# Performance work log

Measured on AMD Instinct MI355X. Metric: run time of the kernel, lower is better.

Reference implementation:

```python
import jax, jax.numpy as jnp
import numpy as np

NEG = -1e6  # masked_softmax fill value from the torch source


def setup_inputs() -> dict:
    key = jax.random.key(0)
    ks = jax.random.split(key, 7)
    B, NQ, NK, D, H = 4, 256, 1024, 256, 256
    queries = jax.random.normal(ks[0], (B, NQ, D), dtype=jnp.float32)
    keys_ = jax.random.normal(ks[1], (B, NK, D), dtype=jnp.float32)
    values = jax.random.normal(ks[2], (B, NK, D), dtype=jnp.float32)
    valid_lens = jax.random.randint(ks[3], (B,), 1, NK + 1, dtype=jnp.int32)
    scale = 1.0 / np.sqrt(D)
    Wq = jax.random.normal(ks[4], (D, H), dtype=jnp.float32) * scale
    Wk = jax.random.normal(ks[5], (D, H), dtype=jnp.float32) * scale
    w_v = jax.random.normal(ks[6], (H,), dtype=jnp.float32) * (1.0 / np.sqrt(H))
    return {"queries": queries, "keys": keys_, "values": values,
            "valid_lens": valid_lens, "Wq": Wq, "Wk": Wk, "w_v": w_v}


def reference(queries, keys, values, valid_lens, Wq, Wk, w_v):
    # projections
    q = jnp.einsum('bqd,dh->bqh', queries, Wq)           # [B,NQ,H]
    k = jnp.einsum('bkd,dh->bkh', keys, Wk)              # [B,NK,H]
    # broadcast-add + tanh + dense(->1): scores [B,NQ,NK]
    features = jnp.tanh(q[:, :, None, :] + k[:, None, :, :])  # [B,NQ,NK,H]
    scores = jnp.einsum('bqkh,h->bqk', features, w_v)
    # masked softmax over last axis with per-batch valid lengths
    nk = keys.shape[1]
    mask = jnp.arange(nk)[None, None, :] < valid_lens[:, None, None]  # [B,1,NK]
    scores = jnp.where(mask, scores, NEG)
    attn = jax.nn.softmax(scores, axis=-1)               # [B,NQ,NK]
    # dropout in eval mode -> identity
    return jnp.einsum('bqk,bkd->bqd', attn, values)      # [B,NQ,D]
```

## Files before the change

kernel.cpp:

```cpp
#include <hip/hip_runtime.h>
#include <hip/hip_fp16.h>
#include <math.h>

#define BB 4
#define NQ 256
#define NK 1024
#define DD 256
#define HH 256

typedef __attribute__((ext_vector_type(8))) _Float16 f16x8;
typedef __attribute__((ext_vector_type(4))) _Float16 f16x4;
typedef __attribute__((ext_vector_type(4))) float f32x4;

__global__ __launch_bounds__(256) void proj_mfma_kernel(
    const float* __restrict__ Q, const float* __restrict__ K,
    const float* __restrict__ Wq, const float* __restrict__ Wk,
    const int* __restrict__ vlen,
    __half* __restrict__ Eq, __half* __restrict__ Ek)
{
    int bx = blockIdx.x;
    int mt = bx >> 3, nt = bx & 7;
    const float *A, *W; __half* C; int bm;
    if (mt < 16) { A = Q; W = Wq; C = Eq; bm = mt * 64; }
    else {
        int kt = mt - 16;
        int b = kt >> 4;
        int lr = (kt & 15) * 64;
        if (lr >= vlen[b]) return;
        A = K; W = Wk; C = Ek; bm = kt * 64;
    }
    int bn = nt * 32;

    __shared__ __half Wt[32][260];

    int tid = threadIdx.x;
    {
        int dp = tid >> 3, cg = tid & 7;
#pragma unroll
        for (int pp = 0; pp < 4; ++pp) {
            int d0r = (dp + pp * 32) * 2;
            float4 r0 = *(const float4*)&W[(size_t)d0r * HH + bn + cg * 4];
            float4 r1 = *(const float4*)&W[(size_t)(d0r + 1) * HH + bn + cg * 4];
            int n = cg * 4;
            *(__half2*)&Wt[n + 0][d0r] = __floats2half2_rn(r0.x, r1.x);
            *(__half2*)&Wt[n + 1][d0r] = __floats2half2_rn(r0.y, r1.y);
            *(__half2*)&Wt[n + 2][d0r] = __floats2half2_rn(r0.z, r1.z);
            *(__half2*)&Wt[n + 3][d0r] = __floats2half2_rn(r0.w, r1.w);
        }
    }
    __syncthreads();

    int lane = tid & 63, w = tid >> 6;
    int wm = w & 1, wn = w >> 1;
    int lm = lane & 15, lk = (lane >> 4) * 4;

    const float* arow0 = A + (size_t)(bm + wm * 32 + lm) * DD;
    const float* arow1 = arow0 + (size_t)16 * DD;
    const __half* brow = &Wt[wn * 16 + lm][0];

    f32x4 acc0 = {0.f, 0.f, 0.f, 0.f};
    f32x4 acc1 = {0.f, 0.f, 0.f, 0.f};

    float4 a00 = *(const float4*)(arow0 + lk);
    float4 a01 = *(const float4*)(arow0 + 16 + lk);
    float4 a10 = *(const float4*)(arow1 + lk);
    float4 a11 = *(const float4*)(arow1 + 16 + lk);
    f16x4 b0 = *(const f16x4*)&brow[lk];
    f16x4 b1 = *(const f16x4*)&brow[16 + lk];

#pragma unroll
    for (int s = 0; s < 8; ++s) {
        float4 c00 = a00, c01 = a01, c10 = a10, c11 = a11;
        f16x4 cb0 = b0, cb1 = b1;
        if (s < 7) {
            int d = (s + 1) * 32;
            a00 = *(const float4*)(arow0 + d + lk);
            a01 = *(const float4*)(arow0 + d + 16 + lk);
            a10 = *(const float4*)(arow1 + d + lk);
            a11 = *(const float4*)(arow1 + d + 16 + lk);
            b0 = *(const f16x4*)&brow[d + lk];
            b1 = *(const f16x4*)&brow[d + 16 + lk];
        }
        f16x8 af0, af1, bf;
        af0[0] = (_Float16)c00.x; af0[1] = (_Float16)c00.y;
        af0[2] = (_Float16)c00.z; af0[3] = (_Float16)c00.w;
        af0[4] = (_Float16)c01.x; af0[5] = (_Float16)c01.y;
        af0[6] = (_Float16)c01.z; af0[7] = (_Float16)c01.w;
        af1[0] = (_Float16)c10.x; af1[1] = (_Float16)c10.y;
        af1[2] = (_Float16)c10.z; af1[3] = (_Float16)c10.w;
        af1[4] = (_Float16)c11.x; af1[5] = (_Float16)c11.y;
        af1[6] = (_Float16)c11.z; af1[7] = (_Float16)c11.w;
        bf[0] = cb0[0]; bf[1] = cb0[1]; bf[2] = cb0[2]; bf[3] = cb0[3];
        bf[4] = cb1[0]; bf[5] = cb1[1]; bf[6] = cb1[2]; bf[7] = cb1[3];
        acc0 = __builtin_amdgcn_mfma_f32_16x16x32_f16(af0, bf, acc0, 0, 0, 0);
        acc1 = __builtin_amdgcn_mfma_f32_16x16x32_f16(af1, bf, acc1, 0, 0, 0);
    }

    int mB0 = bm + wm * 32 + (lane >> 4) * 4;
    int mB1 = mB0 + 16;
    int n = bn + wn * 16 + lm;
#pragma unroll
    for (int r = 0; r < 4; ++r) {
        float e0 = __expf(2.f * fminf(fmaxf(acc0[r], -5.5f), 5.5f));
        float e1 = __expf(2.f * fminf(fmaxf(acc1[r], -5.5f), 5.5f));
        C[(size_t)(mB0 + r) * HH + n] = __float2half(e0);
        C[(size_t)(mB1 + r) * HH + n] = __float2half(e1);
    }
}

__global__ __launch_bounds__(256) void scores_kernel(
    const __half* __restrict__ Eq, const __half* __restrict__ Ek,
    const float* __restrict__ wv, const int* __restrict__ vlen,
    float* __restrict__ P, float* __restrict__ Psum)
{
    __shared__ __align__(16) __half sQ[32][HH + 8];
    __shared__ __align__(16) __half sK[32][HH + 8];
    __shared__ __align__(16) float sW[HH];

    int bid = blockIdx.x;
    int b = bid & 3;
    int rest = bid >> 2;
    int qc = rest & 7;
    int kc = rest >> 3;
    int L = vlen[b];
    int k0 = kc * 32;
    if (k0 >= L) return;
    int q0 = qc * 32;

    int tid = threadIdx.x;
    {
        int c8 = tid & 31;
        int r0 = tid >> 5;
        const __half* gq = Eq + ((size_t)b * NQ + q0) * HH;
        const __half* gk = Ek + ((size_t)b * NK + k0) * HH;
#pragma unroll
        for (int i = 0; i < 4; ++i) {
            int r = r0 + 8 * i;
            *(uint4*)&sQ[r][c8 * 8] = *(const uint4*)&gq[(size_t)r * HH + c8 * 8];
            *(uint4*)&sK[r][c8 * 8] = *(const uint4*)&gk[(size_t)r * HH + c8 * 8];
        }
        sW[tid] = wv[tid];
    }
    __syncthreads();

    int ki = tid & 15, qi = tid >> 4;
    float a00 = 0.f, a01 = 0.f, a10 = 0.f, a11 = 0.f;

#pragma unroll 4
    for (int h4 = 0; h4 < HH / 4; ++h4) {
        float4 w = *(const float4*)&sW[h4 * 4];
        float wxy = w.x + w.y, wzw = w.z + w.w;
        float2 q0a = __half22float2(*(const __half2*)&sQ[qi][h4 * 4]);
        float2 q0b = __half22float2(*(const __half2*)&sQ[qi][h4 * 4 + 2]);
        float2 q1a = __half22float2(*(const __half2*)&sQ[qi + 16][h4 * 4]);
        float2 q1b = __half22float2(*(const __half2*)&sQ[qi + 16][h4 * 4 + 2]);
        float2 k0a = __half22float2(*(const __half2*)&sK[ki][h4 * 4]);
        float2 k0b = __half22float2(*(const __half2*)&sK[ki][h4 * 4 + 2]);
        float2 k1a = __half22float2(*(const __half2*)&sK[ki + 16][h4 * 4]);
        float2 k1b = __half22float2(*(const __half2*)&sK[ki + 16][h4 * 4 + 2]);
        float4 A0 = {q0a.x, q0a.y, q0b.x, q0b.y};
        float4 A1 = {q1a.x, q1a.y, q1b.x, q1b.y};
        float4 B0 = {k0a.x, k0a.y, k0b.x, k0b.y};
        float4 B1 = {k1a.x, k1a.y, k1b.x, k1b.y};
#define QUAD(acc, Aq, Bk)                                                    \
        {                                                                    \
            float E1 = Aq.x * Bk.x, E2 = Aq.y * Bk.y;                        \
            float E3 = Aq.z * Bk.z, E4 = Aq.w * Bk.w;                        \
            float d1 = E1 + 1.f, d2 = E2 + 1.f;                              \
            float d3 = E3 + 1.f, d4 = E4 + 1.f;                              \
            float n12 = fmaf(w.x, E2, fmaf(w.y, E1, wxy));                   \
            float n34 = fmaf(w.z, E4, fmaf(w.w, E3, wzw));                   \
            float d12 = d1 * d2, d34 = d3 * d4;                              \
            float num = fmaf(n12, d34, n34 * d12);                           \
            acc = fmaf(num, __builtin_amdgcn_rcpf(d12 * d34), acc);          \
        }
        QUAD(a00, A0, B0);
        QUAD(a01, A0, B1);
        QUAD(a10, A1, B0);
        QUAD(a11, A1, B1);
#undef QUAD
    }

    int kA = k0 + ki, kB = kA + 16;
    float p00 = (kA < L) ? __expf(-2.f * a00) : 0.f;
    float p10 = (kA < L) ? __expf(-2.f * a10) : 0.f;
    float p01 = (kB < L) ? __expf(-2.f * a01) : 0.f;
    float p11 = (kB < L) ? __expf(-2.f * a11) : 0.f;

    float* s0 = P + ((size_t)b * NQ + q0 + qi) * NK;
    float* s1 = P + ((size_t)b * NQ + q0 + qi + 16) * NK;
    s0[kA] = p00; s0[kB] = p01;
    s1[kA] = p10; s1[kB] = p11;

    float r0s = p00 + p01, r1s = p10 + p11;
#pragma unroll
    for (int o = 1; o <= 8; o <<= 1) {
        r0s += __shfl_xor(r0s, o, 64);
        r1s += __shfl_xor(r1s, o, 64);
    }
    if (ki == 0) {
        Psum[((size_t)b * NQ + q0 + qi) * 32 + kc] = r0s;
        Psum[((size_t)b * NQ + q0 + qi + 16) * 32 + kc] = r1s;
    }
}

__global__ __launch_bounds__(256) void pv_kernel(
    const float* __restrict__ P, const float* __restrict__ V,
    const float* __restrict__ Psum, const int* __restrict__ vlen,
    float* __restrict__ out)
{
    __shared__ __align__(16) float sPt[2][32][36];
    __shared__ __align__(16) float sV[2][32][36];
    __shared__ float sAll[3][64][17];
    __shared__ float sRowsum[32];

    int bid = blockIdx.x;
    int b = bid & 3;
    int rest = bid >> 2;
    int qt = rest >> 3, dt = rest & 7;
    int q0 = qt * 32, d0 = dt * 32;
    int L = vlen[b];
    int nc = (L + 31) >> 5;

    int tid = threadIdx.x;
    if (tid < 32) {
        float s = 0.f;
        const float* pp = Psum + ((size_t)b * NQ + q0 + tid) * 32;
        for (int c = 0; c < nc; ++c) s += pp[c];
        sRowsum[tid] = s;
    }

    int r = tid >> 3, c4 = tid & 7;
    int w = tid >> 6, sp = tid & 63;
    int qg = sp >> 3, dg = sp & 7;

    const float* Pb = P + ((size_t)b * NQ + q0 + r) * NK;
    const float* Vb = V + (size_t)b * NK * DD + d0;

    float4 pf = *(const float4*)(Pb + c4 * 4);
    float4 vf = *(const float4*)(Vb + (size_t)r * DD + c4 * 4);

    float acc[4][4] = {};

    for (int c = 0; c < nc; ++c) {
        int cur = c & 1;
        sPt[cur][c4 * 4 + 0][r] = pf.x;
        sPt[cur][c4 * 4 + 1][r] = pf.y;
        sPt[cur][c4 * 4 + 2][r] = pf.z;
        sPt[cur][c4 * 4 + 3][r] = pf.w;
        *(float4*)&sV[cur][r][c4 * 4] = vf;
        if (c + 1 < nc) {
            int kn = (c + 1) * 32;
            pf = *(const float4*)(Pb + kn + c4 * 4);
            vf = *(const float4*)(Vb + (size_t)(kn + r) * DD + c4 * 4);
        }
        __syncthreads();
#pragma unroll
        for (int kk = 0; kk < 8; ++kk) {
            float4 A  = *(const float4*)&sPt[cur][w * 8 + kk][qg * 4];
            float4 Bv = *(const float4*)&sV[cur][w * 8 + kk][dg * 4];
            acc[0][0] = fmaf(A.x, Bv.x, acc[0][0]);
            acc[0][1] = fmaf(A.x, Bv.y, acc[0][1]);
            acc[0][2] = fmaf(A.x, Bv.z, acc[0][2]);
            acc[0][3] = fmaf(A.x, Bv.w, acc[0][3]);
            acc[1][0] = fmaf(A.y, Bv.x, acc[1][0]);
            acc[1][1] = fmaf(A.y, Bv.y, acc[1][1]);
            acc[1][2] = fmaf(A.y, Bv.z, acc[1][2]);
            acc[1][3] = fmaf(A.y, Bv.w, acc[1][3]);
            acc[2][0] = fmaf(A.z, Bv.x, acc[2][0]);
            acc[2][1] = fmaf(A.z, Bv.y, acc[2][1]);
            acc[2][2] = fmaf(A.z, Bv.z, acc[2][2]);
            acc[2][3] = fmaf(A.z, Bv.w, acc[2][3]);
            acc[3][0] = fmaf(A.w, Bv.x, acc[3][0]);
            acc[3][1] = fmaf(A.w, Bv.y, acc[3][1]);
            acc[3][2] = fmaf(A.w, Bv.z, acc[3][2]);
            acc[3][3] = fmaf(A.w, Bv.w, acc[3][3]);
        }
    }

    if (w > 0) {
#pragma unroll
        for (int i = 0; i < 4; ++i)
#pragma unroll
            for (int j = 0; j < 4; ++j) sAll[w - 1][sp][i * 4 + j] = acc[i][j];
    }
    __syncthreads();
    if (w == 0) {
#pragma unroll
        for (int ww = 0; ww < 3; ++ww)
#pragma unroll
            for (int i = 0; i < 4; ++i)
#pragma unroll
                for (int j = 0; j < 4; ++j) acc[i][j] += sAll[ww][sp][i * 4 + j];
#pragma unroll
        for (int i = 0; i < 4; ++i) {
            float inv = 1.0f / sRowsum[qg * 4 + i];
            float4 o = { acc[i][0] * inv, acc[i][1] * inv,
                         acc[i][2] * inv, acc[i][3] * inv };
            *(float4*)&out[((size_t)b * NQ + q0 + qg * 4 + i) * DD + d0 + dg * 4] = o;
        }
    }
}

extern "C" void kernel_launch(void* const* d_in, const int* in_sizes, int n_in,
                              void* d_out, int out_size, void* d_ws, size_t ws_size,
                              hipStream_t stream) {
    const float* queries = (const float*)d_in[0];
    const float* keys    = (const float*)d_in[1];
    const float* values  = (const float*)d_in[2];
    const int*   vlens   = (const int*)d_in[3];
    const float* Wq      = (const float*)d_in[4];
    const float* Wk      = (const float*)d_in[5];
    const float* wv      = (const float*)d_in[6];
    float* out = (float*)d_out;

    __half* Eqh = (__half*)d_ws;
    __half* Ekh = Eqh + (size_t)BB * NQ * HH;
    float*  P    = (float*)(Ekh + (size_t)BB * NK * HH);
    float*  Psum = P + (size_t)BB * NQ * NK;

    proj_mfma_kernel<<<dim3(640), 256, 0, stream>>>(
        queries, keys, Wq, Wk, vlens, Eqh, Ekh);

    scores_kernel<<<dim3(BB * (NQ / 32) * (NK / 32)), 256, 0, stream>>>(
        Eqh, Ekh, wv, vlens, P, Psum);

    pv_kernel<<<dim3(BB * (NQ / 32) * (DD / 32)), 256, 0, stream>>>(
        P, values, Psum, vlens, out);
}
```

Baseline: 54.93 us.

## Fuse three stages into one cooperative persistent kernel with counter-based dependencies

Replaces the three separate launches (projection, scores, PV) with one cooperative kernel of 1024 blocks. Dependencies between stages are tracked with per-tile atomic counters and spin-waits instead of kernel boundaries. The PV stage is split into four key segments, with partial outputs going to a workspace; the last segment to finish reduces them and normalises. The goal is to cut launch gaps and tail idle time and to spread PV work over more blocks. The cost is an extra memset, spin-wait overhead, an extra partial-output round trip, and reliance on every block being co-resident.

```diff
diff --git a/kernel.cpp b/kernel.cpp
--- a/kernel.cpp
+++ b/kernel.cpp
@@ -7,119 +7,135 @@
 #define NK 1024
 #define DD 256
 #define HH 256
+#define NSEG 4
+#define NBLK 1024
 
 typedef __attribute__((ext_vector_type(8))) _Float16 f16x8;
 typedef __attribute__((ext_vector_type(4))) _Float16 f16x4;
 typedef __attribute__((ext_vector_type(4))) float f32x4;
 
-__global__ __launch_bounds__(256) void proj_mfma_kernel(
+struct SMem {
+    union {
+        struct { __half Wt[32][260]; } p;
+        struct { __half sQ[32][264]; __half sK[32][264]; float sW[HH]; } s;
+        struct { float sPt[2][32][36]; float sV[2][32][36];
+                 float sAll[3][64][17]; float sRowsum[32]; } v;
+    } u;
+};
+
+#define AGENT __HIP_MEMORY_SCOPE_AGENT
+
+__device__ __forceinline__ void dev_proj_tile(
+    int t, SMem& sm, int tid,
     const float* __restrict__ Q, const float* __restrict__ K,
     const float* __restrict__ Wq, const float* __restrict__ Wk,
     const int* __restrict__ vlen,
-    __half* __restrict__ Eq, __half* __restrict__ Ek)
-{
-    int bx = blockIdx.x;
-    int mt = bx >> 3, nt = bx & 7;
+    __half* __restrict__ Eq, __half* __restrict__ Ek, int* projcnt)
+{
+    int mt = t >> 3, nt = t & 7;
     const float *A, *W; __half* C; int bm;
+    bool masked = false;
     if (mt < 16) { A = Q; W = Wq; C = Eq; bm = mt * 64; }
     else {
         int kt = mt - 16;
         int b = kt >> 4;
         int lr = (kt & 15) * 64;
-        if (lr >= vlen[b]) return;
+        masked = (lr >= vlen[b]);
         A = K; W = Wk; C = Ek; bm = kt * 64;
     }
     int bn = nt * 32;
 
-    __shared__ __half Wt[32][260];
-
-    int tid = threadIdx.x;
-    {
-        int dp = tid >> 3, cg = tid & 7;
-#pragma unroll
-        for (int pp = 0; pp < 4; ++pp) {
-            int d0r = (dp + pp * 32) * 2;
-            float4 r0 = *(const float4*)&W[(size_t)d0r * HH + bn + cg * 4];
-            float4 r1 = *(const float4*)&W[(size_t)(d0r + 1) * HH + bn + cg * 4];
-            int n = cg * 4;
-            *(__half2*)&Wt[n + 0][d0r] = __floats2half2_rn(r0.x, r1.x);
-            *(__half2*)&Wt[n + 1][d0r] = __floats2half2_rn(r0.y, r1.y);
-            *(__half2*)&Wt[n + 2][d0r] = __floats2half2_rn(r0.z, r1.z);
-            *(__half2*)&Wt[n + 3][d0r] = __floats2half2_rn(r0.w, r1.w);
-        }
-    }
-    __syncthreads();
-
-    int lane = tid & 63, w = tid >> 6;
-    int wm = w & 1, wn = w >> 1;
-    int lm = lane & 15, lk = (lane >> 4) * 4;
-
-    const float* arow0 = A + (size_t)(bm + wm * 32 + lm) * DD;
-    const float* arow1 = arow0 + (size_t)16 * DD;
-    const __half* brow = &Wt[wn * 16 + lm][0];
-
-    f32x4 acc0 = {0.f, 0.f, 0.f, 0.f};
-    f32x4 acc1 = {0.f, 0.f, 0.f, 0.f};
-
-    float4 a00 = *(const float4*)(arow0 + lk);
-    float4 a01 = *(const float4*)(arow0 + 16 + lk);
-    float4 a10 = *(const float4*)(arow1 + lk);
-    float4 a11 = *(const float4*)(arow1 + 16 + lk);
-    f16x4 b0 = *(const f16x4*)&brow[lk];
-    f16x4 b1 = *(const f16x4*)&brow[16 + lk];
-
-#pragma unroll
-    for (int s = 0; s < 8; ++s) {
-        float4 c00 = a00, c01 = a01, c10 = a10, c11 = a11;
-        f16x4 cb0 = b0, cb1 = b1;
-        if (s < 7) {
-            int d = (s + 1) * 32;
-            a00 = *(const float4*)(arow0 + d + lk);
-            a01 = *(const float4*)(arow0 + d + 16 + lk);
-            a10 = *(const float4*)(arow1 + d + lk);
-            a11 = *(const float4*)(arow1 + d + 16 + lk);
-            b0 = *(const f16x4*)&brow[d + lk];
-            b1 = *(const f16x4*)&brow[d + 16 + lk];
-        }
-        f16x8 af0, af1, bf;
-        af0[0] = (_Float16)c00.x; af0[1] = (_Float16)c00.y;
-        af0[2] = (_Float16)c00.z; af0[3] = (_Float16)c00.w;
-        af0[4] = (_Float16)c01.x; af0[5] = (_Float16)c01.y;
-        af0[6] = (_Float16)c01.z; af0[7] = (_Float16)c01.w;
-        af1[0] = (_Float16)c10.x; af1[1] = (_Float16)c10.y;
-        af1[2] = (_Float16)c10.z; af1[3] = (_Float16)c10.w;
-        af1[4] = (_Float16)c11.x; af1[5] = (_Float16)c11.y;
-        af1[6] = (_Float16)c11.z; af1[7] = (_Float16)c11.w;
-        bf[0] = cb0[0]; bf[1] = cb0[1]; bf[2] = cb0[2]; bf[3] = cb0[3];
-        bf[4] = cb1[0]; bf[5] = cb1[1]; bf[6] = cb1[2]; bf[7] = cb1[3];
-        acc0 = __builtin_amdgcn_mfma_f32_16x16x32_f16(af0, bf, acc0, 0, 0, 0);
-        acc1 = __builtin_amdgcn_mfma_f32_16x16x32_f16(af1, bf, acc1, 0, 0, 0);
-    }
-
-    int mB0 = bm + wm * 32 + (lane >> 4) * 4;
-    int mB1 = mB0 + 16;
-    int n = bn + wn * 16 + lm;
-#pragma unroll
-    for (int r = 0; r < 4; ++r) {
-        float e0 = __expf(2.f * fminf(fmaxf(acc0[r], -5.5f), 5.5f));
-        float e1 = __expf(2.f * fminf(fmaxf(acc1[r], -5.5f), 5.5f));
-        C[(size_t)(mB0 + r) * HH + n] = __float2half(e0);
-        C[(size_t)(mB1 + r) * HH + n] = __float2half(e1);
-    }
-}
-
-__global__ __launch_bounds__(256) void scores_kernel(
+    if (!masked) {
+        auto& Wt = sm.u.p.Wt;
+        {
+            int dp = tid >> 3, cg = tid & 7;
+#pragma unroll
+            for (int pp = 0; pp < 4; ++pp) {
+                int d0r = (dp + pp * 32) * 2;
+                float4 r0 = *(const float4*)&W[(size_t)d0r * HH + bn + cg * 4];
+                float4 r1 = *(const float4*)&W[(size_t)(d0r + 1) * HH + bn + cg * 4];
+                int n = cg * 4;
+                *(__half2*)&Wt[n + 0][d0r] = __floats2half2_rn(r0.x, r1.x);
+                *(__half2*)&Wt[n + 1][d0r] = __floats2half2_rn(r0.y, r1.y);
+                *(__half2*)&Wt[n + 2][d0r] = __floats2half2_rn(r0.z, r1.z);
+                *(__half2*)&Wt[n + 3][d0r] = __floats2half2_rn(r0.w, r1.w);
+            }
+        }
+        __syncthreads();
+
+        int lane = tid & 63, w = tid >> 6;
+        int wm = w & 1, wn = w >> 1;
+        int lm = lane & 15, lk = (lane >> 4) * 4;
+
+        const float* arow0 = A + (size_t)(bm + wm * 32 + lm) * DD;
+        const float* arow1 = arow0 + (size_t)16 * DD;
+        const __half* brow = &Wt[wn * 16 + lm][0];
+
+        f32x4 acc0 = {0.f, 0.f, 0.f, 0.f};
+        f32x4 acc1 = {0.f, 0.f, 0.f, 0.f};
+
+        float4 a00 = *(const float4*)(arow0 + lk);
+        float4 a01 = *(const float4*)(arow0 + 16 + lk);
+        float4 a10 = *(const float4*)(arow1 + lk);
+        float4 a11 = *(const float4*)(arow1 + 16 + lk);
+        f16x4 b0 = *(const f16x4*)&brow[lk];
+        f16x4 b1 = *(const f16x4*)&brow[16 + lk];
+
+#pragma unroll
+        for (int s = 0; s < 8; ++s) {
+            float4 c00 = a00, c01 = a01, c10 = a10, c11 = a11;
+            f16x4 cb0 = b0, cb1 = b1;
+            if (s < 7) {
+                int d = (s + 1) * 32;
+                a00 = *(const float4*)(arow0 + d + lk);
+                a01 = *(const float4*)(arow0 + d + 16 + lk);
+                a10 = *(const float4*)(arow1 + d + lk);
+                a11 = *(const float4*)(arow1 + d + 16 + lk);
+                b0 = *(const f16x4*)&brow[d + lk];
+                b1 = *(const f16x4*)&brow[d + 16 + lk];
+            }
+            f16x8 af0, af1, bf;
+            af0[0] = (_Float16)c00.x; af0[1] = (_Float16)c00.y;
+            af0[2] = (_Float16)c00.z; af0[3] = (_Float16)c00.w;
+            af0[4] = (_Float16)c01.x; af0[5] = (_Float16)c01.y;
+            af0[6] = (_Float16)c01.z; af0[7] = (_Float16)c01.w;
+            af1[0] = (_Float16)c10.x; af1[1] = (_Float16)c10.y;
+            af1[2] = (_Float16)c10.z; af1[3] = (_Float16)c10.w;
+            af1[4] = (_Float16)c11.x; af1[5] = (_Float16)c11.y;
+            af1[6] = (_Float16)c11.z; af1[7] = (_Float16)c11.w;
+            bf[0] = cb0[0]; bf[1] = cb0[1]; bf[2] = cb0[2]; bf[3] = cb0[3];
+            bf[4] = cb1[0]; bf[5] = cb1[1]; bf[6] = cb1[2]; bf[7] = cb1[3];
+            acc0 = __builtin_amdgcn_mfma_f32_16x16x32_f16(af0, bf, acc0, 0, 0, 0);
+            acc1 = __builtin_amdgcn_mfma_f32_16x16x32_f16(af1, bf, acc1, 0, 0, 0);
+        }
+
+        int mB0 = bm + wm * 32 + (lane >> 4) * 4;
+        int mB1 = mB0 + 16;
+        int n = bn + wn * 16 + lm;
+#pragma unroll
+        for (int r = 0; r < 4; ++r) {
+            float e0 = __expf(2.f * fminf(fmaxf(acc0[r], -5.5f), 5.5f));
+            float e1 = __expf(2.f * fminf(fmaxf(acc1[r], -5.5f), 5.5f));
+            C[(size_t)(mB0 + r) * HH + n] = __float2half(e0);
+            C[(size_t)(mB1 + r) * HH + n] = __float2half(e1);
+        }
+    }
+    if (projcnt) {
+        __syncthreads();
+        if (tid == 0)
+            __hip_atomic_fetch_add(&projcnt[mt], 1, __ATOMIC_RELEASE, AGENT);
+    }
+}
+
+__device__ __forceinline__ void dev_scores_tile(
+    int t, SMem& sm, int tid,
     const __half* __restrict__ Eq, const __half* __restrict__ Ek,
     const float* __restrict__ wv, const int* __restrict__ vlen,
-    float* __restrict__ P, float* __restrict__ Psum)
-{
-    __shared__ __align__(16) __half sQ[32][HH + 8];
-    __shared__ __align__(16) __half sK[32][HH + 8];
-    __shared__ __align__(16) float sW[HH];
-
-    int bid = blockIdx.x;
-    int b = bid & 3;
-    int rest = bid >> 2;
+    float* __restrict__ P, float* __restrict__ Psum,
+    int* projcnt, int* scnt)
+{
+    int b = t & 3;
+    int rest = t >> 2;
     int qc = rest & 7;
     int kc = rest >> 3;
     int L = vlen[b];
@@ -127,7 +143,21 @@
     if (k0 >= L) return;
     int q0 = qc * 32;
 
-    int tid = threadIdx.x;
+    if (projcnt) {
+        if (tid == 0) {
+            int mtq = b * 4 + (qc >> 1);
+            int mtk = 16 + b * 16 + (kc >> 1);
+            while (__hip_atomic_load(&projcnt[mtq], __ATOMIC_ACQUIRE, AGENT) < 8)
+                __builtin_amdgcn_s_sleep(16);
+            while (__hip_atomic_load(&projcnt[mtk], __ATOMIC_ACQUIRE, AGENT) < 8)
+                __builtin_amdgcn_s_sleep(16);
+        }
+        __syncthreads();
+    }
+
+    auto& sQ = sm.u.s.sQ;
+    auto& sK = sm.u.s.sK;
+    auto& sW = sm.u.s.sW;
     {
         int c8 = tid & 31;
         int r0 = tid >> 5;
@@ -202,33 +232,38 @@
         Psum[((size_t)b * NQ + q0 + qi) * 32 + kc] = r0s;
         Psum[((size_t)b * NQ + q0 + qi + 16) * 32 + kc] = r1s;
     }
-}
-
-__global__ __launch_bounds__(256) void pv_kernel(
+
+    if (scnt) {
+        __syncthreads();
+        if (tid == 0)
+            __hip_atomic_fetch_add(&scnt[b * 8 + qc], 1, __ATOMIC_RELEASE, AGENT);
+    }
+}
+
+__device__ __forceinline__ void dev_pv_seg(
+    int t, SMem& sm, int tid,
     const float* __restrict__ P, const float* __restrict__ V,
     const float* __restrict__ Psum, const int* __restrict__ vlen,
-    float* __restrict__ out)
-{
-    __shared__ __align__(16) float sPt[2][32][36];
-    __shared__ __align__(16) float sV[2][32][36];
-    __shared__ float sAll[3][64][17];
-    __shared__ float sRowsum[32];
-
-    int bid = blockIdx.x;
-    int b = bid & 3;
-    int rest = bid >> 2;
-    int qt = rest >> 3, dt = rest & 7;
+    float* __restrict__ Opart, float* __restrict__ out,
+    int* scnt, int* segcnt, int* sflag)
+{
+    int b = t & 3;
+    int qt = (t >> 2) & 7, dt = (t >> 5) & 7, seg = t >> 8;
     int q0 = qt * 32, d0 = dt * 32;
     int L = vlen[b];
     int nc = (L + 31) >> 5;
 
-    int tid = threadIdx.x;
-    if (tid < 32) {
-        float s = 0.f;
-        const float* pp = Psum + ((size_t)b * NQ + q0 + tid) * 32;
-        for (int c = 0; c < nc; ++c) s += pp[c];
-        sRowsum[tid] = s;
-    }
+    if (tid == 0) {
+        while (__hip_atomic_load(&scnt[b * 8 + qt], __ATOMIC_ACQUIRE, AGENT) < nc)
+            __builtin_amdgcn_s_sleep(16);
+    }
+    __syncthreads();
+
+    int c0 = (nc * seg) / NSEG, c1 = (nc * (seg + 1)) / NSEG;
+
+    auto& sPt = sm.u.v.sPt;
+    auto& sV  = sm.u.v.sV;
+    auto& sAll = sm.u.v.sAll;
 
     int r = tid >> 3, c4 = tid & 7;
     int w = tid >> 6, sp = tid & 63;
@@ -237,19 +272,20 @@
     const float* Pb = P + ((size_t)b * NQ + q0 + r) * NK;
     const float* Vb = V + (size_t)b * NK * DD + d0;
 
-    float4 pf = *(const float4*)(Pb + c4 * 4);
-    float4 vf = *(const float4*)(Vb + (size_t)r * DD + c4 * 4);
+    int cld = (c0 < c1) ? c0 : 0;
+    float4 pf = *(const float4*)(Pb + cld * 32 + c4 * 4);
+    float4 vf = *(const float4*)(Vb + (size_t)(cld * 32 + r) * DD + c4 * 4);
 
     float acc[4][4] = {};
 
-    for (int c = 0; c < nc; ++c) {
+    for (int c = c0; c < c1; ++c) {
         int cur = c & 1;
         sPt[cur][c4 * 4 + 0][r] = pf.x;
         sPt[cur][c4 * 4 + 1][r] = pf.y;
         sPt[cur][c4 * 4 + 2][r] = pf.z;
         sPt[cur][c4 * 4 + 3][r] = pf.w;
         *(float4*)&sV[cur][r][c4 * 4] = vf;
-        if (c + 1 < nc) {
+        if (c + 1 < c1) {
             int kn = (c + 1) * 32;
             pf = *(const float4*)(Pb + kn + c4 * 4);
             vf = *(const float4*)(Vb + (size_t)(kn + r) * DD + c4 * 4);
@@ -278,6 +314,186 @@
         }
     }
 
+    __syncthreads();
+    if (w > 0) {
+#pragma unroll
+        for (int i = 0; i < 4; ++i)
+#pragma unroll
+            for (int j = 0; j < 4; ++j) sAll[w - 1][sp][i * 4 + j] = acc[i][j];
+    }
+    __syncthreads();
+    if (w == 0) {
+#pragma unroll
+        for (int ww = 0; ww < 3; ++ww)
+#pragma unroll
+            for (int i = 0; i < 4; ++i)
+#pragma unroll
+                for (int j = 0; j < 4; ++j) acc[i][j] += sAll[ww][sp][i * 4 + j];
+        float* op = Opart + (size_t)seg * (BB * NQ * DD);
+#pragma unroll
+        for (int i = 0; i < 4; ++i) {
+            float4 o = { acc[i][0], acc[i][1], acc[i][2], acc[i][3] };
+            *(float4*)&op[((size_t)b * NQ + q0 + qg * 4 + i) * DD + d0 + dg * 4] = o;
+        }
+    }
+
+    __syncthreads();
+    if (tid == 0) {
+        int old = __hip_atomic_fetch_add(&segcnt[t & 255], 1,
+                                         __ATOMIC_ACQ_REL, AGENT);
+        *sflag = old;
+    }
+    __syncthreads();
+    if (*sflag == NSEG - 1) {
+        auto& sRowsum = sm.u.v.sRowsum;
+        if (tid < 32) {
+            float s = 0.f;
+            const float* pp = Psum + ((size_t)b * NQ + q0 + tid) * 32;
+            for (int c = 0; c < nc; ++c) s += pp[c];
+            sRowsum[tid] = s;
+        }
+        __syncthreads();
+        int qi = tid >> 3, cc = tid & 7;
+        const size_t SEGSZ = (size_t)BB * NQ * DD;
+        size_t off = ((size_t)b * NQ + q0 + qi) * DD + d0 + cc * 4;
+        float4 o = {0.f, 0.f, 0.f, 0.f};
+#pragma unroll
+        for (int s = 0; s < NSEG; ++s) {
+            float4 x = *(const float4*)&Opart[s * SEGSZ + off];
+            o.x += x.x; o.y += x.y; o.z += x.z; o.w += x.w;
+        }
+        float inv = 1.0f / sRowsum[qi];
+        o.x *= inv; o.y *= inv; o.z *= inv; o.w *= inv;
+        *(float4*)&out[off] = o;
+    }
+}
+
+__global__ __launch_bounds__(256, 4) void fused_all(
+    const float* __restrict__ queries, const float* __restrict__ keys,
+    const float* __restrict__ values, const int* __restrict__ vlen,
+    const float* __restrict__ Wq, const float* __restrict__ Wk,
+    const float* __restrict__ wv, float* __restrict__ out,
+    __half* __restrict__ Eqh, __half* __restrict__ Ekh,
+    float* __restrict__ P, float* __restrict__ Psum,
+    float* __restrict__ Opart, int* __restrict__ flags)
+{
+    __shared__ SMem sm;
+    __shared__ int sflag;
+    int tid = threadIdx.x;
+    int bid = blockIdx.x;
+
+    int* projcnt = flags;
+    int* scnt    = flags + 128;
+    int* segcnt  = flags + 256;
+
+    if (bid < 640)
+        dev_proj_tile(bid, sm, tid, queries, keys, Wq, Wk, vlen,
+                      Eqh, Ekh, projcnt);
+    __syncthreads();
+
+    dev_scores_tile(bid, sm, tid, Eqh, Ekh, wv, vlen, P, Psum,
+                    projcnt, scnt);
+    __syncthreads();
+
+    dev_pv_seg(bid, sm, tid, P, values, Psum, vlen, Opart, out,
+               scnt, segcnt, &sflag);
+}
+
+__global__ __launch_bounds__(256) void proj_sa(
+    const float* __restrict__ Q, const float* __restrict__ K,
+    const float* __restrict__ Wq, const float* __restrict__ Wk,
+    const int* __restrict__ vlen, __half* __restrict__ Eq,
+    __half* __restrict__ Ek)
+{
+    __shared__ SMem sm;
+    dev_proj_tile(blockIdx.x, sm, threadIdx.x, Q, K, Wq, Wk, vlen,
+                  Eq, Ek, nullptr);
+}
+
+__global__ __launch_bounds__(256) void scores_sa(
+    const __half* __restrict__ Eq, const __half* __restrict__ Ek,
+    const float* __restrict__ wv, const int* __restrict__ vlen,
+    float* __restrict__ P, float* __restrict__ Psum)
+{
+    __shared__ SMem sm;
+    dev_scores_tile(blockIdx.x, sm, threadIdx.x, Eq, Ek, wv, vlen, P, Psum,
+                    nullptr, nullptr);
+}
+
+__global__ __launch_bounds__(256) void pv_sa(
+    const float* __restrict__ P, const float* __restrict__ V,
+    const float* __restrict__ Psum, const int* __restrict__ vlen,
+    float* __restrict__ out)
+{
+    __shared__ __align__(16) float sPt[2][32][36];
+    __shared__ __align__(16) float sV[2][32][36];
+    __shared__ float sAll[3][64][17];
+    __shared__ float sRowsum[32];
+
+    int bid = blockIdx.x;
+    int b = bid & 3;
+    int rest = bid >> 2;
+    int qt = rest >> 3, dt = rest & 7;
+    int q0 = qt * 32, d0 = dt * 32;
+    int L = vlen[b];
+    int nc = (L + 31) >> 5;
+
+    int tid = threadIdx.x;
+    if (tid < 32) {
+        float s = 0.f;
+        const float* pp = Psum + ((size_t)b * NQ + q0 + tid) * 32;
+        for (int c = 0; c < nc; ++c) s += pp[c];
+        sRowsum[tid] = s;
+    }
+
+    int r = tid >> 3, c4 = tid & 7;
+    int w = tid >> 6, sp = tid & 63;
+    int qg = sp >> 3, dg = sp & 7;
+
+    const float* Pb = P + ((size_t)b * NQ + q0 + r) * NK;
+    const float* Vb = V + (size_t)b * NK * DD + d0;
+
+    float4 pf = *(const float4*)(Pb + c4 * 4);
+    float4 vf = *(const float4*)(Vb + (size_t)r * DD + c4 * 4);
+
+    float acc[4][4] = {};
+
+    for (int c = 0; c < nc; ++c) {
+        int cur = c & 1;
+        sPt[cur][c4 * 4 + 0][r] = pf.x;
+        sPt[cur][c4 * 4 + 1][r] = pf.y;
+        sPt[cur][c4 * 4 + 2][r] = pf.z;
+        sPt[cur][c4 * 4 + 3][r] = pf.w;
+        *(float4*)&sV[cur][r][c4 * 4] = vf;
+        if (c + 1 < nc) {
+            int kn = (c + 1) * 32;
+            pf = *(const float4*)(Pb + kn + c4 * 4);
+            vf = *(const float4*)(Vb + (size_t)(kn + r) * DD + c4 * 4);
+        }
+        __syncthreads();
+#pragma unroll
+        for (int kk = 0; kk < 8; ++kk) {
+            float4 A  = *(const float4*)&sPt[cur][w * 8 + kk][qg * 4];
+            float4 Bv = *(const float4*)&sV[cur][w * 8 + kk][dg * 4];
+            acc[0][0] = fmaf(A.x, Bv.x, acc[0][0]);
+            acc[0][1] = fmaf(A.x, Bv.y, acc[0][1]);
+            acc[0][2] = fmaf(A.x, Bv.z, acc[0][2]);
+            acc[0][3] = fmaf(A.x, Bv.w, acc[0][3]);
+            acc[1][0] = fmaf(A.y, Bv.x, acc[1][0]);
+            acc[1][1] = fmaf(A.y, Bv.y, acc[1][1]);
+            acc[1][2] = fmaf(A.y, Bv.z, acc[1][2]);
+            acc[1][3] = fmaf(A.y, Bv.w, acc[1][3]);
+            acc[2][0] = fmaf(A.z, Bv.x, acc[2][0]);
+            acc[2][1] = fmaf(A.z, Bv.y, acc[2][1]);
+            acc[2][2] = fmaf(A.z, Bv.z, acc[2][2]);
+            acc[2][3] = fmaf(A.z, Bv.w, acc[2][3]);
+            acc[3][0] = fmaf(A.w, Bv.x, acc[3][0]);
+            acc[3][1] = fmaf(A.w, Bv.y, acc[3][1]);
+            acc[3][2] = fmaf(A.w, Bv.z, acc[3][2]);
+            acc[3][3] = fmaf(A.w, Bv.w, acc[3][3]);
+        }
+    }
+
     if (w > 0) {
 #pragma unroll
         for (int i = 0; i < 4; ++i)
@@ -314,17 +530,28 @@
     const float* wv      = (const float*)d_in[6];
     float* out = (float*)d_out;
 
-    __half* Eqh = (__half*)d_ws;
-    __half* Ekh = Eqh + (size_t)BB * NQ * HH;
-    float*  P    = (float*)(Ekh + (size_t)BB * NK * HH);
-    float*  Psum = P + (size_t)BB * NQ * NK;
-
-    proj_mfma_kernel<<<dim3(640), 256, 0, stream>>>(
-        queries, keys, Wq, Wk, vlens, Eqh, Ekh);
-
-    scores_kernel<<<dim3(BB * (NQ / 32) * (NK / 32)), 256, 0, stream>>>(
-        Eqh, Ekh, wv, vlens, P, Psum);
-
-    pv_kernel<<<dim3(BB * (NQ / 32) * (DD / 32)), 256, 0, stream>>>(
-        P, values, Psum, vlens, out);
-}
+    int*    flags = (int*)d_ws;
+    __half* Eqh   = (__half*)((char*)d_ws + 4096);
+    __half* Ekh   = Eqh + (size_t)BB * NQ * HH;
+    float*  P     = (float*)(Ekh + (size_t)BB * NK * HH);
+    float*  Psum  = P + (size_t)BB * NQ * NK;
+    float*  Opart = Psum + (size_t)BB * NQ * 32;
+
+    hipMemsetAsync(flags, 0, 4096, stream);
+
+    void* args[] = { (void*)&queries, (void*)&keys, (void*)&values,
+                     (void*)&vlens, (void*)&Wq, (void*)&Wk, (void*)&wv,
+                     (void*)&out, (void*)&Eqh, (void*)&Ekh, (void*)&P,
+                     (void*)&Psum, (void*)&Opart, (void*)&flags };
+    hipError_t e = hipLaunchCooperativeKernel((void*)fused_all,
+                                              dim3(NBLK), dim3(256),
+                                              args, 0, stream);
+    if (e != hipSuccess) {
+        proj_sa<<<dim3(640), 256, 0, stream>>>(queries, keys, Wq, Wk, vlens,
+                                               Eqh, Ekh);
+        scores_sa<<<dim3(BB * (NQ / 32) * (NK / 32)), 256, 0, stream>>>(
+            Eqh, Ekh, wv, vlens, P, Psum);
+        pv_sa<<<dim3(BB * (NQ / 32) * (DD / 32)), 256, 0, stream>>>(
+            P, values, Psum, vlens, out);
+    }
+}
```

Result: slower. 199.4 us (+263.0%).

## Simplify score rational-tanh math and halve PV query tile to double blocks

Applied to the files above, without the earlier changes.

The score loop now computes each pair of tanh terms directly from fma-built denominators with one reciprocal per pair, instead of one reciprocal per quad with extra products. The PV kernel tile shrinks from 32 to 16 query rows, doubling the grid to 512 blocks for better CU occupancy. Loading is split: half the threads load P and half load V. Per-thread accumulators drop from 16 to 8. The cost is twice as many reciprocals in the score loop, and each V tile is reloaded by twice as many blocks.

```diff
diff --git a/kernel.cpp b/kernel.cpp
--- a/kernel.cpp
+++ b/kernel.cpp
@@ -149,7 +149,6 @@
 #pragma unroll 4
     for (int h4 = 0; h4 < HH / 4; ++h4) {
         float4 w = *(const float4*)&sW[h4 * 4];
-        float wxy = w.x + w.y, wzw = w.z + w.w;
         float2 q0a = __half22float2(*(const __half2*)&sQ[qi][h4 * 4]);
         float2 q0b = __half22float2(*(const __half2*)&sQ[qi][h4 * 4 + 2]);
         float2 q1a = __half22float2(*(const __half2*)&sQ[qi + 16][h4 * 4]);
@@ -162,23 +161,22 @@
         float4 A1 = {q1a.x, q1a.y, q1b.x, q1b.y};
         float4 B0 = {k0a.x, k0a.y, k0b.x, k0b.y};
         float4 B1 = {k1a.x, k1a.y, k1b.x, k1b.y};
-#define QUAD(acc, Aq, Bk)                                                    \
+#define PAIR4(acc, Aq, Bk)                                                   \
         {                                                                    \
-            float E1 = Aq.x * Bk.x, E2 = Aq.y * Bk.y;                        \
-            float E3 = Aq.z * Bk.z, E4 = Aq.w * Bk.w;                        \
-            float d1 = E1 + 1.f, d2 = E2 + 1.f;                              \
-            float d3 = E3 + 1.f, d4 = E4 + 1.f;                              \
-            float n12 = fmaf(w.x, E2, fmaf(w.y, E1, wxy));                   \
-            float n34 = fmaf(w.z, E4, fmaf(w.w, E3, wzw));                   \
-            float d12 = d1 * d2, d34 = d3 * d4;                              \
-            float num = fmaf(n12, d34, n34 * d12);                           \
-            acc = fmaf(num, __builtin_amdgcn_rcpf(d12 * d34), acc);          \
-        }
-        QUAD(a00, A0, B0);
-        QUAD(a01, A0, B1);
-        QUAD(a10, A1, B0);
-        QUAD(a11, A1, B1);
-#undef QUAD
+            float d1 = fmaf(Aq.x, Bk.x, 1.f);                                \
+            float d2 = fmaf(Aq.y, Bk.y, 1.f);                                \
+            float n12 = fmaf(w.y, d1, w.x * d2);                             \
+            acc = fmaf(n12, __builtin_amdgcn_rcpf(d1 * d2), acc);            \
+            float d3 = fmaf(Aq.z, Bk.z, 1.f);                                \
+            float d4 = fmaf(Aq.w, Bk.w, 1.f);                                \
+            float n34 = fmaf(w.w, d3, w.z * d4);                             \
+            acc = fmaf(n34, __builtin_amdgcn_rcpf(d3 * d4), acc);            \
+        }
+        PAIR4(a00, A0, B0);
+        PAIR4(a01, A0, B1);
+        PAIR4(a10, A1, B0);
+        PAIR4(a11, A1, B1);
+#undef PAIR4
     }
 
     int kA = k0 + ki, kB = kA + 16;
@@ -209,55 +207,70 @@
     const float* __restrict__ Psum, const int* __restrict__ vlen,
     float* __restrict__ out)
 {
-    __shared__ __align__(16) float sPt[2][32][36];
+    __shared__ __align__(16) float sPt[2][32][18];
     __shared__ __align__(16) float sV[2][32][36];
-    __shared__ float sAll[3][64][17];
-    __shared__ float sRowsum[32];
+    __shared__ float sAll[3][64][9];
+    __shared__ float sRowsum[16];
 
     int bid = blockIdx.x;
     int b = bid & 3;
     int rest = bid >> 2;
     int qt = rest >> 3, dt = rest & 7;
-    int q0 = qt * 32, d0 = dt * 32;
+    int q0 = qt * 16, d0 = dt * 32;
     int L = vlen[b];
     int nc = (L + 31) >> 5;
 
     int tid = threadIdx.x;
-    if (tid < 32) {
+    if (tid < 16) {
         float s = 0.f;
         const float* pp = Psum + ((size_t)b * NQ + q0 + tid) * 32;
         for (int c = 0; c < nc; ++c) s += pp[c];
         sRowsum[tid] = s;
     }
 
-    int r = tid >> 3, c4 = tid & 7;
+    bool isP = tid < 128;
+    int pr = tid >> 3, pc4 = tid & 7;
+    int vt = tid & 127;
+    int vr = vt >> 2, vc = (vt & 3) * 2;
+
     int w = tid >> 6, sp = tid & 63;
     int qg = sp >> 3, dg = sp & 7;
 
-    const float* Pb = P + ((size_t)b * NQ + q0 + r) * NK;
+    const float* Pb = P + ((size_t)b * NQ + q0 + pr) * NK;
     const float* Vb = V + (size_t)b * NK * DD + d0;
 
-    float4 pf = *(const float4*)(Pb + c4 * 4);
-    float4 vf = *(const float4*)(Vb + (size_t)r * DD + c4 * 4);
-
-    float acc[4][4] = {};
+    float4 pf = {0,0,0,0}, vfa = {0,0,0,0}, vfb = {0,0,0,0};
+    if (isP) pf = *(const float4*)(Pb + pc4 * 4);
+    else {
+        vfa = *(const float4*)(Vb + (size_t)vr * DD + vc * 4);
+        vfb = *(const float4*)(Vb + (size_t)vr * DD + vc * 4 + 4);
+    }
+
+    float acc[2][4] = {};
 
     for (int c = 0; c < nc; ++c) {
         int cur = c & 1;
-        sPt[cur][c4 * 4 + 0][r] = pf.x;
-        sPt[cur][c4 * 4 + 1][r] = pf.y;
-        sPt[cur][c4 * 4 + 2][r] = pf.z;
-        sPt[cur][c4 * 4 + 3][r] = pf.w;
-        *(float4*)&sV[cur][r][c4 * 4] = vf;
+        if (isP) {
+            sPt[cur][pc4 * 4 + 0][pr] = pf.x;
+            sPt[cur][pc4 * 4 + 1][pr] = pf.y;
+            sPt[cur][pc4 * 4 + 2][pr] = pf.z;
+            sPt[cur][pc4 * 4 + 3][pr] = pf.w;
+        } else {
+            *(float4*)&sV[cur][vr][vc * 4] = vfa;
+            *(float4*)&sV[cur][vr][vc * 4 + 4] = vfb;
+        }
         if (c + 1 < nc) {
             int kn = (c + 1) * 32;
-            pf = *(const float4*)(Pb + kn + c4 * 4);
-            vf = *(const float4*)(Vb + (size_t)(kn + r) * DD + c4 * 4);
+            if (isP) pf = *(const float4*)(Pb + kn + pc4 * 4);
+            else {
+                vfa = *(const float4*)(Vb + (size_t)(kn + vr) * DD + vc * 4);
+                vfb = *(const float4*)(Vb + (size_t)(kn + vr) * DD + vc * 4 + 4);
+            }
         }
         __syncthreads();
 #pragma unroll
         for (int kk = 0; kk < 8; ++kk) {
-            float4 A  = *(const float4*)&sPt[cur][w * 8 + kk][qg * 4];
+            float2 A  = *(const float2*)&sPt[cur][w * 8 + kk][qg * 2];
             float4 Bv = *(const float4*)&sV[cur][w * 8 + kk][dg * 4];
             acc[0][0] = fmaf(A.x, Bv.x, acc[0][0]);
             acc[0][1] = fmaf(A.x, Bv.y, acc[0][1]);
@@ -267,20 +280,12 @@
             acc[1][1] = fmaf(A.y, Bv.y, acc[1][1]);
             acc[1][2] = fmaf(A.y, Bv.z, acc[1][2]);
             acc[1][3] = fmaf(A.y, Bv.w, acc[1][3]);
-            acc[2][0] = fmaf(A.z, Bv.x, acc[2][0]);
-            acc[2][1] = fmaf(A.z, Bv.y, acc[2][1]);
-            acc[2][2] = fmaf(A.z, Bv.z, acc[2][2]);
-            acc[2][3] = fmaf(A.z, Bv.w, acc[2][3]);
-            acc[3][0] = fmaf(A.w, Bv.x, acc[3][0]);
-            acc[3][1] = fmaf(A.w, Bv.y, acc[3][1]);
-            acc[3][2] = fmaf(A.w, Bv.z, acc[3][2]);
-            acc[3][3] = fmaf(A.w, Bv.w, acc[3][3]);
         }
     }
 
     if (w > 0) {
 #pragma unroll
-        for (int i = 0; i < 4; ++i)
+        for (int i = 0; i < 2; ++i)
 #pragma unroll
             for (int j = 0; j < 4; ++j) sAll[w - 1][sp][i * 4 + j] = acc[i][j];
     }
@@ -289,15 +294,15 @@
 #pragma unroll
         for (int ww = 0; ww < 3; ++ww)
 #pragma unroll
-            for (int i = 0; i < 4; ++i)
+            for (int i = 0; i < 2; ++i)
 #pragma unroll
                 for (int j = 0; j < 4; ++j) acc[i][j] += sAll[ww][sp][i * 4 + j];
 #pragma unroll
-        for (int i = 0; i < 4; ++i) {
-            float inv = 1.0f / sRowsum[qg * 4 + i];
+        for (int i = 0; i < 2; ++i) {
+            float inv = 1.0f / sRowsum[qg * 2 + i];
             float4 o = { acc[i][0] * inv, acc[i][1] * inv,
                          acc[i][2] * inv, acc[i][3] * inv };
-            *(float4*)&out[((size_t)b * NQ + q0 + qg * 4 + i) * DD + d0 + dg * 4] = o;
+            *(float4*)&out[((size_t)b * NQ + q0 + qg * 2 + i) * DD + d0 + dg * 4] = o;
         }
     }
 }
@@ -325,6 +330,6 @@
     scores_kernel<<<dim3(BB * (NQ / 32) * (NK / 32)), 256, 0, stream>>>(
         Eqh, Ekh, wv, vlens, P, Psum);
 
-    pv_kernel<<<dim3(BB * (NQ / 32) * (DD / 32)), 256, 0, stream>>>(
+    pv_kernel<<<dim3(BB * (NQ / 16) * (DD / 32)), 256, 0, stream>>>(
         P, values, Psum, vlens, out);
 }
```

After: 52.85 us, median of 2. 1.04x faster.
